# Kernel optimization log

Measured on AMD Instinct MI355X. Metric: run time of the kernel, lower is better.

## Reference

```python
import jax, jax.numpy as jnp
import numpy as np

B, N, D, H = 8, 4096, 256, 4
KP, KN = N // 16, N // 32
EPS = 1e-6

def _ln(x, g, b):
    m = jnp.mean(x, -1, keepdims=True)
    v = jnp.var(x, -1, keepdims=True)
    return (x - m) / jnp.sqrt(v + 1e-5) * g + b

def _cross_attn(q_in, kv_in, wq, wk, wv, wo, bo):
    # q_in [1,Nq,D], kv_in [1,Nk,D]
    Bq, Nq, Dm = q_in.shape
    Nk = kv_in.shape[1]
    dh = Dm // H
    q = (q_in @ wq).reshape(Bq, Nq, H, dh).transpose(0, 2, 1, 3)
    k = (kv_in @ wk).reshape(Bq, Nk, H, dh).transpose(0, 2, 1, 3)
    v = (kv_in @ wv).reshape(Bq, Nk, H, dh).transpose(0, 2, 1, 3)
    attn = jax.nn.softmax(jnp.einsum('bhqd,bhkd->bhqk', q, k) * (dh ** -0.5), axis=-1)
    out = jnp.einsum('bhqk,bhkd->bhqd', attn, v).transpose(0, 2, 1, 3).reshape(Bq, Nq, Dm)
    return out @ wo + bo

def setup_inputs():
    key = jax.random.key(0)
    ks = jax.random.split(key, 40)
    f32 = jnp.float32
    def w(i, shape, s):
        return s * jax.random.normal(ks[i], shape, f32)
    inp = {}
    inp['x'] = jax.random.normal(ks[0], (B, N, D), f32)
    inp['mask'] = (jax.random.randint(ks[1], (B, N), 0, 3) - 1).astype(jnp.int32)  # values in {-1,0,1}
    inp['pos_emb'] = 0.02 * jax.random.normal(ks[2], (1, N, D), f32)
    inp['sim_p_w'] = w(3, (D, D), 0.2); inp['sim_p_b'] = jnp.zeros((D,), f32)
    inp['sim_n_w'] = w(4, (D, D), 0.2); inp['sim_n_b'] = jnp.zeros((D,), f32)
    inp['adj_w'] = w(5, (D, D), 0.05)
    inp['gnn_p_w1'] = w(6, (D, D), 0.05); inp['gnn_p_w2'] = w(7, (D, D), 0.05)
    inp['gnn_n_w1'] = w(8, (D, D), 0.05); inp['gnn_n_w2'] = w(9, (D, D), 0.05)
    for i in range(1, 6):
        inp['ln%d_g' % i] = jnp.ones((D,), f32)
        inp['ln%d_b' % i] = jnp.zeros((D,), f32)
    names = ['i2q_wq', 'i2q_wk', 'i2q_wv', 'i2q_wo', 'q2i_wq', 'q2i_wk', 'q2i_wv', 'q2i_wo']
    for j, nme in enumerate(names):
        inp[nme] = w(10 + j, (D, D), 0.05)
    inp['i2q_bo'] = jnp.zeros((D,), f32)
    inp['q2i_bo'] = jnp.zeros((D,), f32)
    inp['mlp_w'] = w(20, (D, D), 0.05); inp['mlp_b'] = jnp.zeros((D,), f32)
    inp['g_i2t'] = 0.1 * jax.random.normal(ks[21], (1, 1, D), f32)
    inp['g_t2i'] = 0.1 * jax.random.normal(ks[22], (1, 1, D), f32)
    return inp

def reference(x, mask, pos_emb, sim_p_w, sim_p_b, sim_n_w, sim_n_b, adj_w,
              gnn_p_w1, gnn_p_w2, gnn_n_w1, gnn_n_w2,
              ln1_g, ln1_b, ln2_g, ln2_b, ln3_g, ln3_b, ln4_g, ln4_b, ln5_g, ln5_b,
              i2q_wq, i2q_wk, i2q_wv, i2q_wo, i2q_bo,
              q2i_wq, q2i_wk, q2i_wv, q2i_wo, q2i_bo,
              mlp_w, mlp_b, g_i2t, g_t2i):
    pos_mask = (mask == 1).astype(x.dtype)[..., None]    # [B,N,1]
    neg_mask = (mask == -1).astype(x.dtype)[..., None]
    pos_query = (x * pos_mask).sum(1, keepdims=True) / (pos_mask.sum(1, keepdims=True) + EPS)  # [B,1,D]
    neg_query = (x * neg_mask).sum(1, keepdims=True) / (neg_mask.sum(1, keepdims=True) + EPS)
    pos_sim = jax.nn.sigmoid(((x @ sim_p_w + sim_p_b) * pos_query).sum(-1))  # [B,N]
    neg_sim = jax.nn.sigmoid(((x @ sim_n_w + sim_n_b) * neg_query).sum(-1))
    weight_p, idx_p = jax.lax.top_k(pos_sim, KP)
    weight_n, idx_n = jax.lax.top_k(neg_sim, KN)
    scale = 1.0 / jnp.sqrt(jnp.asarray(D, x.dtype))

    def gcn(node, w1, w2):
        adj = jax.nn.softmax((node @ adj_w) @ node.T * scale, axis=-1)  # [K,K]
        h = jax.nn.relu(adj @ (node @ w1))
        return adj @ (h @ w2)

    def batch_forward(ip, wp, inn, wn, feat):
        node_p = feat[ip] * (wp > 0.6).astype(feat.dtype)[:, None]       # [KP,D]
        query_p = gcn(node_p, gnn_p_w1, gnn_p_w2) + pos_emb[0, ip]
        node_n = feat[inn] * (wn > 0.6).astype(feat.dtype)[:, None]      # [KN,D]
        query_n = gcn(node_n, gnn_n_w1, gnn_n_w2) + pos_emb[0, inn]
        query = jnp.concatenate([query_p, query_n], 0)[None]             # [1,KP+KN,D]
        featb = feat[None]                                               # [1,N,D]
        query = query + g_i2t * _cross_attn(_ln(query, ln1_g, ln1_b), _ln(featb, ln2_g, ln2_b),
                                            i2q_wq, i2q_wk, i2q_wv, i2q_wo, i2q_bo)
        featb = featb + g_t2i * _cross_attn(_ln(featb, ln3_g, ln3_b), _ln(query, ln4_g, ln4_b),
                                            q2i_wq, q2i_wk, q2i_wv, q2i_wo, q2i_bo)
        featb = featb + (_ln(featb, ln5_g, ln5_b) @ mlp_w + mlp_b)
        return featb

    out = jax.vmap(batch_forward)(idx_p, weight_p, idx_n, weight_n, x)   # [B,1,N,D]
    return out, pos_sim, neg_sim
```

## Files before the change

kernel.cpp:

```cpp
#include <hip/hip_runtime.h>

#define BB 8
#define NN 4096
#define DD 256
#define HH 4
#define DHH 64
#define KPP 256
#define KNN 128
#define SCH 64

typedef float f32x4 __attribute__((ext_vector_type(4)));
typedef short bf16x8 __attribute__((ext_vector_type(8)));
typedef short bf16x4 __attribute__((ext_vector_type(4)));

#define FLAG_TRANSB 1
#define FLAG_RELU   2

__device__ __forceinline__ float bf2f(unsigned short u){
  union { unsigned int i; float f; } v; v.i = ((unsigned int)u) << 16; return v.f;
}
__device__ __forceinline__ unsigned short f2bf(float f){
  union { float f; unsigned int i; } v; v.f = f;
  return (unsigned short)((v.i + 0x7FFFu + ((v.i >> 16) & 1u)) >> 16);
}
__device__ __forceinline__ void gload16(const void* g, void* l){
  __builtin_amdgcn_global_load_lds((const __attribute__((address_space(1))) void*)g,
                                   (__attribute__((address_space(3))) void*)l, 16, 0, 0);
}

__global__ __launch_bounds__(256) void stats_part(const float* __restrict__ x,
                                                  const int* __restrict__ mask,
                                                  float* __restrict__ part,
                                                  float* __restrict__ pcnt){
  int b = blockIdx.y, c = blockIdx.x, t = threadIdx.x;
  int w = t >> 6, lane = t & 63;
  const int R = NN / SCH;
  int n0 = c * R;
  const float* xb = x + ((long)b*NN + n0)*DD;
  const int* mb = mask + (long)b*NN + n0;
  float4 sp = {0.f,0.f,0.f,0.f}, sn = {0.f,0.f,0.f,0.f};
  int cp = 0, cn = 0;
  #pragma unroll 4
  for (int r = w; r < R; r += 4){
    int mv = mb[r];
    float4 v = ((const float4*)(xb + (long)r*DD))[lane];
    if (mv == 1){ sp.x += v.x; sp.y += v.y; sp.z += v.z; sp.w += v.w; cp++; }
    else if (mv == -1){ sn.x += v.x; sn.y += v.y; sn.z += v.z; sn.w += v.w; cn++; }
  }
  __shared__ float red[2][4][256];
  __shared__ int cnt[2][4];
  ((float4*)&red[0][w][0])[lane] = sp;
  ((float4*)&red[1][w][0])[lane] = sn;
  if (lane == 0){ cnt[0][w] = cp; cnt[1][w] = cn; }
  __syncthreads();
  float s0 = red[0][0][t]+red[0][1][t]+red[0][2][t]+red[0][3][t];
  float s1 = red[1][0][t]+red[1][1][t]+red[1][2][t]+red[1][3][t];
  part[(((long)(b*SCH+c)*2+0)*DD)+t] = s0;
  part[(((long)(b*SCH+c)*2+1)*DD)+t] = s1;
  if (t == 0){
    pcnt[(b*SCH+c)*2+0] = (float)(cnt[0][0]+cnt[0][1]+cnt[0][2]+cnt[0][3]);
    pcnt[(b*SCH+c)*2+1] = (float)(cnt[1][0]+cnt[1][1]+cnt[1][2]+cnt[1][3]);
  }
}

__global__ void stats_vec(const float* __restrict__ part, const float* __restrict__ pcnt,
                          const float* __restrict__ Wp, const float* __restrict__ bp,
                          const float* __restrict__ Wn, const float* __restrict__ bn,
                          float* __restrict__ vvec, float* __restrict__ cscal){
  int b = blockIdx.x, k = threadIdx.x;
  __shared__ float qp[256], qn[256], red[256];
  {
    float sp=0.f, sn=0.f, cp=0.f, cn=0.f;
    for (int c = 0; c < SCH; c++){
      sp += part[(((long)(b*SCH+c)*2+0)*DD)+k];
      sn += part[(((long)(b*SCH+c)*2+1)*DD)+k];
      cp += pcnt[(b*SCH+c)*2+0];
      cn += pcnt[(b*SCH+c)*2+1];
    }
    qp[k] = sp / (cp + 1e-6f);
    qn[k] = sn / (cn + 1e-6f);
  }
  __syncthreads();
  float vp = 0.f, vn = 0.f;
  for (int j = 0; j < DD; j++){ vp += Wp[(long)k*DD+j]*qp[j]; vn += Wn[(long)k*DD+j]*qn[j]; }
  vvec[(long)(b*2+0)*DD+k] = vp; vvec[(long)(b*2+1)*DD+k] = vn;
  red[k] = bp[k]*qp[k];
  __syncthreads();
  for (int s = 128; s > 0; s >>= 1){ if (k < s) red[k] += red[k+s]; __syncthreads(); }
  if (k == 0) cscal[b*2+0] = red[0];
  __syncthreads();
  red[k] = bn[k]*qn[k];
  __syncthreads();
  for (int s = 128; s > 0; s >>= 1){ if (k < s) red[k] += red[k+s]; __syncthreads(); }
  if (k == 0) cscal[b*2+1] = red[0];
}

__global__ void sim_norm_kernel(const float* __restrict__ x, const float* __restrict__ vvec,
                                const float* __restrict__ cscal,
                                float* __restrict__ simP, float* __restrict__ simN,
                                unsigned short* __restrict__ xhat){
  int b = blockIdx.y;
  int w = threadIdx.x >> 6, lane = threadIdx.x & 63;
  int n = blockIdx.x*4 + w;
  long row = (long)b*NN + n;
  const float4* xr = (const float4*)(x + row*DD);
  float4 xv = xr[lane];
  float4 a = ((const float4*)(vvec + (long)(b*2+0)*DD))[lane];
  float4 c = ((const float4*)(vvec + (long)(b*2+1)*DD))[lane];
  float sp = xv.x*a.x + xv.y*a.y + xv.z*a.z + xv.w*a.w;
  float sn = xv.x*c.x + xv.y*c.y + xv.z*c.z + xv.w*c.w;
  float s  = xv.x+xv.y+xv.z+xv.w;
  float q  = xv.x*xv.x+xv.y*xv.y+xv.z*xv.z+xv.w*xv.w;
  for (int off = 32; off; off >>= 1){
    sp += __shfl_xor(sp, off); sn += __shfl_xor(sn, off);
    s  += __shfl_xor(s, off);  q  += __shfl_xor(q, off);
  }
  float m = s*(1.f/256.f);
  float var = q*(1.f/256.f) - m*m;
  float rinv = rsqrtf(var + 1e-5f);
  ushort4 o;
  o.x = f2bf((xv.x-m)*rinv); o.y = f2bf((xv.y-m)*rinv);
  o.z = f2bf((xv.z-m)*rinv); o.w = f2bf((xv.w-m)*rinv);
  ((ushort4*)(xhat + row*DD))[lane] = o;
  if (lane == 0){
    float zp = sp + cscal[b*2+0], zn = sn + cscal[b*2+1];
    simP[row] = 1.f/(1.f+expf(-zp));
    simN[row] = 1.f/(1.f+expf(-zn));
  }
}

__global__ __launch_bounds__(256) void topk_radix(const float* __restrict__ simP,
                                                  const float* __restrict__ simN,
                                                  const float* __restrict__ x,
                                                  int* __restrict__ idxb, float* __restrict__ wb,
                                                  float* __restrict__ node){
  __shared__ unsigned int vals[4096];
  __shared__ unsigned int hist[4096];
  __shared__ unsigned short eql[4096];
  __shared__ unsigned int tsum[256];
  __shared__ unsigned int sB, sRem, sCG, sCnt, sEq;
  int id = blockIdx.x; int sgn = id & 1, b = id >> 1;
  int K = (sgn == 0) ? KPP : KNN;
  const float* s = (sgn == 0 ? simP : simN) + (long)b*NN;
  int t = threadIdx.x;
  if (t == 0){ sCG = 0; sCnt = 0; sEq = 0; }
  for (int i = t; i < 4096; i += 256){ vals[i] = __float_as_uint(s[i]); hist[i] = 0; }
  __syncthreads();

  auto find_thresh = [&](int NB, unsigned need){
    int per = NB >> 8;
    int base = t*per;
    unsigned local = 0;
    for (int j = 0; j < per; j++) local += hist[base+j];
    tsum[t] = local;
    __syncthreads();
    #pragma unroll
    for (int st = 1; st < 256; st <<= 1){
      unsigned v = (t + st < 256) ? tsum[t+st] : 0u;
      __syncthreads();
      tsum[t] += v;
      __syncthreads();
    }
    unsigned after = (t < 255) ? tsum[t+1] : 0u;
    if (after < need && after + local >= need){
      unsigned c = after;
      for (int j = per-1; j >= 0; j--){
        unsigned h = hist[base+j];
        c += h;
        if (c >= need){
          sB = (unsigned)(base+j);
          sRem = need - (c - h);
          atomicAdd(&sCG, c - h);
          break;
        }
      }
    }
    __syncthreads();
  };

  for (int i = t; i < 4096; i += 256) atomicAdd(&hist[vals[i] >> 20], 1u);
  __syncthreads();
  find_thresh(4096, (unsigned)K);
  unsigned B1 = sB, rem1 = sRem;
  __syncthreads();
  for (int i = t; i < 4096; i += 256) hist[i] = 0;
  __syncthreads();
  for (int i = t; i < 4096; i += 256){
    unsigned v = vals[i];
    if ((v >> 20) == B1) atomicAdd(&hist[(v >> 8) & 0xFFFu], 1u);
  }
  __syncthreads();
  find_thresh(4096, rem1);
  unsigned B2 = sB, rem2 = sRem;
  unsigned pre = (B1 << 12) | B2;
  __syncthreads();
  hist[t] = 0;
  __syncthreads();
  for (int i = t; i < 4096; i += 256){
    unsigned v = vals[i];
    if ((v >> 8) == pre) atomicAdd(&hist[v & 0xFFu], 1u);
  }
  __syncthreads();
  find_thresh(256, rem2);
  unsigned T = (pre << 8) | sB;
  unsigned cg = sCG;
  __syncthreads();
  hist[t] = 0;
  __syncthreads();

  int* oi = idxb + (long)id*256;
  float* ow = wb + (long)id*256;
  for (int i = t; i < 4096; i += 256){
    unsigned v = vals[i];
    if (v > T){
      unsigned p = atomicAdd(&sCnt, 1u);
      oi[p] = i; ow[p] = __uint_as_float(v);
      hist[p] = (unsigned)i; hist[256+p] = v;
    }
    else if (v == T){ unsigned e = atomicAdd(&sEq, 1u); eql[e] = (unsigned short)i; }
  }
  __syncthreads();
  int ne = K - (int)cg;
  int eqn = (int)sEq;
  for (int e = t; e < eqn; e += 256){
    int myi = eql[e]; int r = 0;
    for (int e2 = 0; e2 < eqn; e2++) r += (eql[e2] < myi);
    if (r < ne){
      oi[cg + r] = myi; ow[cg + r] = __uint_as_float(T);
      hist[cg + r] = (unsigned)myi; hist[256 + cg + r] = T;
    }
  }
  __syncthreads();
  int rbase = (sgn == 0) ? 0 : KPP;
  int lane = t & 63, rw = t >> 6;
  for (int i0 = 0; i0 < K; i0 += 4){
    int r = i0 + rw;
    int idx = (int)hist[r];
    float wv = __uint_as_float(hist[256 + r]);
    float4 vsel;
    if (wv > 0.6f) vsel = ((const float4*)(x + ((long)b*NN + idx)*DD))[lane];
    else vsel = (float4){0.f,0.f,0.f,0.f};
    ((float4*)(node + ((long)b*384 + rbase + r)*DD))[lane] = vsel;
  }
}

__global__ void softmax_dual(float* __restrict__ A0, int L0, int rpb0, long bs0, int rows0,
                             float* __restrict__ A1, int L1, int rpb1, long bs1, int rows1){
  int w = threadIdx.x >> 6, lane = threadIdx.x & 63;
  long row = (long)blockIdx.x*4 + w;
  float* A; int L, rpb; long bs;
  if (row < rows0){ A = A0; L = L0; rpb = rpb0; bs = bs0; }
  else { row -= rows0; if (row >= rows1) return; A = A1; L = L1; rpb = rpb1; bs = bs1; }
  int b = (int)(row / rpb), r = (int)(row % rpb);
  float* a = A + (long)b*bs + (long)r*L;
  int e = L >> 6;
  float vals[4]; float mx = -1e30f;
  for (int j = 0; j < e; j++){ vals[j] = a[lane*e+j]; mx = fmaxf(mx, vals[j]); }
  for (int off = 32; off; off >>= 1) mx = fmaxf(mx, __shfl_xor(mx, off));
  float sum = 0.f;
  for (int j = 0; j < e; j++){ vals[j] = expf(vals[j]-mx); sum += vals[j]; }
  for (int off = 32; off; off >>= 1) sum += __shfl_xor(sum, off);
  float rinv = 1.f/sum;
  for (int j = 0; j < e; j++) a[lane*e+j] = vals[j]*rinv;
}

__global__ void rownorm_kernel(const float* __restrict__ X, unsigned short* __restrict__ Y, int rows){
  int w = threadIdx.x >> 6, lane = threadIdx.x & 63;
  long row = (long)blockIdx.x*4 + w;
  if (row >= rows) return;
  const float4* xr = (const float4*)(X + row*DD);
  float4 xv = xr[lane];
  float s = xv.x+xv.y+xv.z+xv.w;
  float q = xv.x*xv.x+xv.y*xv.y+xv.z*xv.z+xv.w*xv.w;
  for (int off = 32; off; off >>= 1){ s += __shfl_xor(s, off); q += __shfl_xor(q, off); }
  float m = s*(1.f/256.f);
  float var = q*(1.f/256.f) - m*m;
  float rinv = rsqrtf(var + 1e-5f);
  ushort4 o;
  o.x = f2bf((xv.x-m)*rinv); o.y = f2bf((xv.y-m)*rinv);
  o.z = f2bf((xv.z-m)*rinv); o.w = f2bf((xv.w-m)*rinv);
  ((ushort4*)(Y + row*DD))[lane] = o;
}

struct FoldArgs { const float* W[9]; const float* g[9]; unsigned short* BT[9]; float sc[9]; };
struct BiasArgs { const float* W[7]; const float* b[7]; const float* addb[7]; float* out[7]; float sc[7]; };

__global__ void fold_w(FoldArgs fa){
  int m = blockIdx.y, tile = blockIdx.x, t = threadIdx.x;
  const float* W = fa.W[m]; const float* g = fa.g[m]; unsigned short* BT = fa.BT[m];
  float sc = fa.sc[m];
  __shared__ float T[64][65];
  int tn = (tile & 3)*64, tk = (tile >> 2)*64;
  #pragma unroll 4
  for (int p = 0; p < 16; p++){
    int kl = p*4 + (t >> 6), nl = t & 63;
    float v = W[(long)(tk+kl)*256 + tn + nl];
    if (g) v *= g[tk+kl];
    T[kl][nl] = v * sc;
  }
  __syncthreads();
  #pragma unroll 4
  for (int p = 0; p < 16; p++){
    int nl = p*4 + (t >> 6), kl = t & 63;
    BT[(long)(tn+nl)*256 + tk + kl] = f2bf(T[kl][nl]);
  }
}

__global__ void fold_b(BiasArgs ba){
  int m = blockIdx.x, n = threadIdx.x;
  const float* W = ba.W[m]; const float* b = ba.b[m];
  float s = (ba.addb[m] != nullptr) ? ba.addb[m][n] : 0.f;
  for (int k = 0; k < 256; k++) s += b[k]*W[(long)k*256+n];
  ba.out[m][n] = s * ba.sc[m];
}

struct GP {
  const float* A; long sAb; int lda;
  const float* B; long sBb; int ldb;
  float* C; long sCb; int ldc;
  const int* pidx; const float* pe;
  int M, N, K; float alpha; int flags;
};
struct GP4 { GP p[4]; };

__global__ __launch_bounds__(256) void gemm_multi(GP4 g4){
  GP p = g4.p[blockIdx.z >> 3];
  int b = blockIdx.z & 7;
  int m0 = blockIdx.y*64, n0 = blockIdx.x*64;
  if (m0 >= p.M || n0 >= p.N) return;
  __shared__ __align__(16) unsigned short As[64*40];
  __shared__ __align__(16) unsigned short Bs[64*40];
  const float* Ab = p.A + (long)b*p.sAb;
  const float* Bb = p.B + (long)b*p.sBb;
  int t = threadIdx.x;
  int w = t >> 6, lane = t & 63, lrowi = lane & 15, lquad = lane >> 4;
  int wm = w >> 1, wn = w & 1;
  f32x4 acc[2][2];
  #pragma unroll
  for (int i = 0; i < 2; i++)
    #pragma unroll
    for (int j = 0; j < 2; j++) acc[i][j] = (f32x4){0.f,0.f,0.f,0.f};
  int am = t >> 2, akq = t & 3;
  for (int k0 = 0; k0 < p.K; k0 += 32){
    {
      const float4* s4 = (const float4*)(Ab + (long)(m0+am)*p.lda + k0 + akq*8);
      float4 u = s4[0], vv = s4[1];
      unsigned short tmp[8];
      tmp[0]=f2bf(u.x); tmp[1]=f2bf(u.y); tmp[2]=f2bf(u.z); tmp[3]=f2bf(u.w);
      tmp[4]=f2bf(vv.x); tmp[5]=f2bf(vv.y); tmp[6]=f2bf(vv.z); tmp[7]=f2bf(vv.w);
      *(uint4*)(&As[am*40 + akq*8]) = *(uint4*)tmp;
    }
    if (p.flags & FLAG_TRANSB){
      const float4* s4 = (const float4*)(Bb + (long)(n0+am)*p.ldb + k0 + akq*8);
      float4 u = s4[0], vv = s4[1];
      unsigned short tmp[8];
      tmp[0]=f2bf(u.x); tmp[1]=f2bf(u.y); tmp[2]=f2bf(u.z); tmp[3]=f2bf(u.w);
      tmp[4]=f2bf(vv.x); tmp[5]=f2bf(vv.y); tmp[6]=f2bf(vv.z); tmp[7]=f2bf(vv.w);
      *(uint4*)(&Bs[am*40 + akq*8]) = *(uint4*)tmp;
    } else {
      int bn = t & 63, bkb = (t >> 6)*8;
      #pragma unroll
      for (int j = 0; j < 8; j++)
        Bs[bn*40 + bkb + j] = f2bf(Bb[(long)(k0+bkb+j)*p.ldb + n0 + bn]);
    }
    __syncthreads();
    bf16x8 af[2], bfr[2];
    #pragma unroll
    for (int i = 0; i < 2; i++)
      af[i] = *(const bf16x8*)(&As[(wm*32 + i*16 + lrowi)*40 + lquad*8]);
    #pragma unroll
    for (int j = 0; j < 2; j++)
      bfr[j] = *(const bf16x8*)(&Bs[(wn*32 + j*16 + lrowi)*40 + lquad*8]);
    #pragma unroll
    for (int i = 0; i < 2; i++)
      #pragma unroll
      for (int j = 0; j < 2; j++)
        acc[i][j] = __builtin_amdgcn_mfma_f32_16x16x32_bf16(af[i], bfr[j], acc[i][j], 0, 0, 0);
    __syncthreads();
  }
  float* Cb = p.C + (long)b*p.sCb;
  #pragma unroll
  for (int i = 0; i < 2; i++)
    #pragma unroll
    for (int j = 0; j < 2; j++){
      int col = n0 + wn*32 + j*16 + lrowi;
      #pragma unroll
      for (int r = 0; r < 4; r++){
        int row = m0 + wm*32 + i*16 + lquad*4 + r;
        float v = p.alpha*acc[i][j][r];
        if (p.flags & FLAG_RELU) v = fmaxf(v, 0.f);
        if (p.pidx != nullptr){
          int idx = p.pidx[b*512 + row];
          v += p.pe[(long)idx*256 + col];
        }
        Cb[(long)row*p.ldc + col] = v;
      }
    }
}

template<typename OT, bool RES, bool GATE>
__global__ __launch_bounds__(256) void gemm128(
    const unsigned short* __restrict__ A, long sAb,
    const unsigned short* __restrict__ BT,
    OT* __restrict__ C, long sCb, int ldc,
    const float* __restrict__ R, long sRb,
    const float* __restrict__ bias, const float* __restrict__ gate)
{
  __shared__ __align__(16) unsigned short As[4096];
  __shared__ __align__(16) unsigned short Bs[4096];
  int t = threadIdx.x;
  int w = t >> 6, lane = t & 63, lrowi = lane & 15, lquad = lane >> 4;
  int wm = w >> 1, wn = w & 1;
  int m0 = blockIdx.y*128, n0 = blockIdx.x*128;
  const unsigned short* Ab = A + (long)blockIdx.z*sAb + (long)m0*256;
  const unsigned short* Bb = BT + (long)n0*256;
  int g0 = t, g1 = 256 + t;
  int row0 = g0 >> 2, kq0 = g0 & 3;
  int row1 = g1 >> 2, kq1 = g1 & 3;
  f32x4 acc[4][4];
  #pragma unroll
  for (int i = 0; i < 4; i++)
    #pragma unroll
    for (int j = 0; j < 4; j++) acc[i][j] = (f32x4){0.f,0.f,0.f,0.f};

  for (int k0 = 0; k0 < 256; k0 += 32){
    gload16(Ab + (long)row0*256 + k0 + kq0*8, &As[g0*8]);
    gload16(Ab + (long)row1*256 + k0 + kq1*8, &As[g1*8]);
    gload16(Bb + (long)row0*256 + k0 + kq0*8, &Bs[g0*8]);
    gload16(Bb + (long)row1*256 + k0 + kq1*8, &Bs[g1*8]);
    __syncthreads();
    bf16x8 af[4], bfr[4];
    #pragma unroll
    for (int i = 0; i < 4; i++)
      af[i] = *(const bf16x8*)(&As[((wm*64 + i*16 + lrowi)*4 + lquad)*8]);
    #pragma unroll
    for (int j = 0; j < 4; j++)
      bfr[j] = *(const bf16x8*)(&Bs[((wn*64 + j*16 + lrowi)*4 + lquad)*8]);
    #pragma unroll
    for (int i = 0; i < 4; i++)
      #pragma unroll
      for (int j = 0; j < 4; j++)
        acc[i][j] = __builtin_amdgcn_mfma_f32_16x16x32_bf16(af[i], bfr[j], acc[i][j], 0, 0, 0);
    __syncthreads();
  }
  OT* Cb = C + (long)blockIdx.z*sCb;
  const float* Rb = RES ? (R + (long)blockIdx.z*sRb) : nullptr;
  #pragma unroll
  for (int j = 0; j < 4; j++){
    int col = n0 + wn*64 + j*16 + lrowi;
    float bv = bias[col];
    float gv = GATE ? gate[col] : 1.f;
    #pragma unroll
    for (int i = 0; i < 4; i++){
      #pragma unroll
      for (int r = 0; r < 4; r++){
        int row = m0 + wm*64 + i*16 + lquad*4 + r;
        float v = acc[i][j][r] + bv;
        if (GATE) v *= gv;
        if (RES) v += Rb[(long)row*256 + col];
        if constexpr (sizeof(OT) == 4) Cb[(long)row*ldc + col] = v;
        else                           Cb[(long)row*ldc + col] = f2bf(v);
      }
    }
  }
}

template<int NFRAG>
__global__ __launch_bounds__(256) void flash_kernel(
    const unsigned short* __restrict__ Q, long sQb, int ldq,
    const unsigned short* __restrict__ Kt, const unsigned short* __restrict__ Vt,
    long sKb, int ldkv,
    unsigned short* __restrict__ O, long sOb,
    float* __restrict__ Opart, float* __restrict__ Lpart,
    int Nq, int Nk, int nsplit)
{
  __shared__ __align__(16) unsigned short Kl[32*72];
  __shared__ __align__(16) unsigned short Vl[64*36];
  __shared__ __align__(16) unsigned short Pl[4*NFRAG*16*36];
  int b = blockIdx.z, h = blockIdx.y;
  int nqg = Nq / (64*NFRAG);
  int qg = blockIdx.x % nqg, split = blockIdx.x / nqg;
  int kchunk = Nk / nsplit;
  int kbeg = split*kchunk, kend = kbeg + kchunk;
  int t = threadIdx.x, w = t >> 6, lane = t & 63, lrowi = lane & 15, lquad = lane >> 4;
  int q0 = qg*(64*NFRAG) + w*(16*NFRAG);
  const unsigned short* Qb = Q + (long)b*sQb + h*DHH;
  const unsigned short* Kb = Kt + (long)b*sKb + h*DHH;
  const unsigned short* Vb = Vt + (long)b*sKb + h*DHH;
  bf16x8 qa[NFRAG][2];
  #pragma unroll
  for (int f = 0; f < NFRAG; f++)
    #pragma unroll
    for (int kt = 0; kt < 2; kt++)
      qa[f][kt] = *(const bf16x8*)(Qb + (long)(q0 + f*16 + lrowi)*ldq + kt*32 + lquad*8);

  f32x4 o[NFRAG][4];
  float psum[NFRAG][4];
  #pragma unroll
  for (int f = 0; f < NFRAG; f++)
    #pragma unroll
    for (int cj = 0; cj < 4; cj++){
      o[f][cj] = (f32x4){0.f,0.f,0.f,0.f};
      psum[f][cj] = 0.f;
    }
  int skq = t >> 3, sdq = (t & 7)*8;
  int skrow = ((skq & 1) << 4) | (skq >> 1);
  int vkq = t & 31, vdq = (t >> 5)*8;
  unsigned short* Pw = &Pl[w*(NFRAG*16*36)];

  for (int kt0 = kbeg; kt0 < kend; kt0 += 32){
    {
      uint4 kv = *(const uint4*)(Kb + (long)(kt0+skq)*ldkv + sdq);
      *(uint4*)(&Kl[skrow*72 + sdq]) = kv;
      uint4 vv = *(const uint4*)(Vb + (long)(kt0+vkq)*ldkv + vdq);
      const unsigned short* vp = (const unsigned short*)&vv;
      #pragma unroll
      for (int j = 0; j < 8; j++) Vl[(vdq+j)*36 + vkq] = vp[j];
    }
    __syncthreads();
    bf16x8 kb0 = *(const bf16x8*)(&Kl[(0*16+lrowi)*72 + lquad*8]);
    bf16x8 kb1 = *(const bf16x8*)(&Kl[(0*16+lrowi)*72 + 32 + lquad*8]);
    bf16x8 kb2 = *(const bf16x8*)(&Kl[(1*16+lrowi)*72 + lquad*8]);
    bf16x8 kb3 = *(const bf16x8*)(&Kl[(1*16+lrowi)*72 + 32 + lquad*8]);
    union { bf16x8 v8; bf16x4 v4[2]; } vbu[4];
    #pragma unroll
    for (int cj = 0; cj < 4; cj++){
      const unsigned short* vb = &Vl[(cj*16+lrowi)*36 + lquad*8];
      vbu[cj].v4[0] = *(const bf16x4*)vb;
      vbu[cj].v4[1] = *(const bf16x4*)(vb + 4);
    }
    #pragma unroll
    for (int f = 0; f < NFRAG; f++){
      f32x4 S0 = (f32x4){0.f,0.f,0.f,0.f}, S1 = (f32x4){0.f,0.f,0.f,0.f};
      S0 = __builtin_amdgcn_mfma_f32_16x16x32_bf16(qa[f][0], kb0, S0, 0, 0, 0);
      S0 = __builtin_amdgcn_mfma_f32_16x16x32_bf16(qa[f][1], kb1, S0, 0, 0, 0);
      S1 = __builtin_amdgcn_mfma_f32_16x16x32_bf16(qa[f][0], kb2, S1, 0, 0, 0);
      S1 = __builtin_amdgcn_mfma_f32_16x16x32_bf16(qa[f][1], kb3, S1, 0, 0, 0);
      unsigned short* Pf = Pw + f*(16*36);
      #pragma unroll
      for (int r = 0; r < 4; r++){
        float p0 = exp2f(S0[r]);
        float p1 = exp2f(S1[r]);
        psum[f][r] += p0 + p1;
        unsigned int pk;
        asm("v_cvt_pk_bf16_f32 %0, %1, %2" : "=v"(pk) : "v"(p0), "v"(p1));
        *(unsigned int*)(&Pf[(lquad*4+r)*36 + 2*lrowi]) = pk;
      }
    }
    __asm__ volatile("s_waitcnt lgkmcnt(0)" ::: "memory");
    #pragma unroll
    for (int f = 0; f < NFRAG; f++){
      const unsigned short* pp = &Pw[f*(16*36) + lrowi*36 + lquad*8];
      union { bf16x8 v8; bf16x4 v4[2]; } pa;
      pa.v4[0] = *(const bf16x4*)pp;
      pa.v4[1] = *(const bf16x4*)(pp + 4);
      #pragma unroll
      for (int cj = 0; cj < 4; cj++)
        o[f][cj] = __builtin_amdgcn_mfma_f32_16x16x32_bf16(pa.v8, vbu[cj].v8, o[f][cj], 0, 0, 0);
    }
    __syncthreads();
  }
  float lsum[NFRAG][4];
  #pragma unroll
  for (int f = 0; f < NFRAG; f++)
    #pragma unroll
    for (int r = 0; r < 4; r++){
      float s = psum[f][r];
      #pragma unroll
      for (int off = 1; off < 16; off <<= 1) s += __shfl_xor(s, off);
      lsum[f][r] = s;
    }
  if (nsplit > 1){
    int p = (b*HH + h)*nsplit + split;
    float* Op = Opart + (long)p*Nq*DHH;
    #pragma unroll
    for (int f = 0; f < NFRAG; f++)
      #pragma unroll
      for (int r = 0; r < 4; r++){
        int row = q0 + f*16 + lquad*4 + r;
        #pragma unroll
        for (int cj = 0; cj < 4; cj++)
          Op[(long)row*DHH + cj*16 + lrowi] = o[f][cj][r];
        if (lrowi == 0) Lpart[(long)p*Nq + row] = lsum[f][r];
      }
  } else {
    unsigned short* Ob = O + (long)b*sOb + h*DHH;
    #pragma unroll
    for (int f = 0; f < NFRAG; f++)
      #pragma unroll
      for (int r = 0; r < 4; r++){
        float rl = 1.f/lsum[f][r];
        int row = q0 + f*16 + lquad*4 + r;
        #pragma unroll
        for (int cj = 0; cj < 4; cj++)
          Ob[(long)row*DD + cj*16 + lrowi] = f2bf(o[f][cj][r]*rl);
      }
  }
}

__global__ void flash_combine(const float* __restrict__ Opart, const float* __restrict__ Lpart,
                              unsigned short* __restrict__ O, long sOb, int Nq, int nsplit){
  int gr = blockIdx.x*4 + (threadIdx.x >> 6);
  int d = threadIdx.x & 63;
  int bh = gr / Nq, row = gr % Nq;
  float accO = 0.f, accL = 0.f;
  for (int s = 0; s < nsplit; s++){
    long p = (long)bh*nsplit + s;
    accL += Lpart[p*Nq + row];
    accO += Opart[(p*Nq + row)*DHH + d];
  }
  int b = bh / HH, h = bh % HH;
  O[(long)b*sOb + (long)row*DD + h*DHH + d] = f2bf(accO/accL);
}

extern "C" void kernel_launch(void* const* d_in, const int* in_sizes, int n_in,
                              void* d_out, int out_size, void* d_ws, size_t ws_size,
                              hipStream_t stream) {
  (void)in_sizes; (void)n_in; (void)out_size; (void)ws_size;
  const float* x        = (const float*)d_in[0];
  const int*   mask     = (const int*)d_in[1];
  const float* pos_emb  = (const float*)d_in[2];
  const float* sim_p_w  = (const float*)d_in[3];
  const float* sim_p_b  = (const float*)d_in[4];
  const float* sim_n_w  = (const float*)d_in[5];
  const float* sim_n_b  = (const float*)d_in[6];
  const float* adj_w    = (const float*)d_in[7];
  const float* gnn_p_w1 = (const float*)d_in[8];
  const float* gnn_p_w2 = (const float*)d_in[9];
  const float* gnn_n_w1 = (const float*)d_in[10];
  const float* gnn_n_w2 = (const float*)d_in[11];
  const float* ln1_g = (const float*)d_in[12]; const float* ln1_b = (const float*)d_in[13];
  const float* ln2_g = (const float*)d_in[14]; const float* ln2_b = (const float*)d_in[15];
  const float* ln3_g = (const float*)d_in[16]; const float* ln3_b = (const float*)d_in[17];
  const float* ln4_g = (const float*)d_in[18]; const float* ln4_b = (const float*)d_in[19];
  const float* ln5_g = (const float*)d_in[20]; const float* ln5_b = (const float*)d_in[21];
  const float* i2q_wq = (const float*)d_in[22];
  const float* i2q_wk = (const float*)d_in[23];
  const float* i2q_wv = (const float*)d_in[24];
  const float* i2q_wo = (const float*)d_in[25];
  const float* q2i_wq = (const float*)d_in[26];
  const float* q2i_wk = (const float*)d_in[27];
  const float* q2i_wv = (const float*)d_in[28];
  const float* q2i_wo = (const float*)d_in[29];
  const float* i2q_bo = (const float*)d_in[30];
  const float* q2i_bo = (const float*)d_in[31];
  const float* mlp_w  = (const float*)d_in[32];
  const float* mlp_b  = (const float*)d_in[33];
  const float* g_i2t  = (const float*)d_in[34];
  const float* g_t2i  = (const float*)d_in[35];

  float* out  = (float*)d_out;
  float* simP = out + (size_t)BB*NN*DD;
  float* simN = simP + (size_t)BB*NN;

  char* w8 = (char*)d_ws;
  size_t off = 0;
  auto take = [&](size_t bytes)->void*{
    void* p = (void*)(w8 + off);
    off += (bytes + 255) & ~(size_t)255;
    return p;
  };
  float* part   = (float*)take((size_t)BB*SCH*2*DD*4);
  float* pcnt   = (float*)take((size_t)BB*SCH*2*4);
  float* vvec   = (float*)take((size_t)BB*2*DD*4);
  float* cscal  = (float*)take((size_t)BB*2*4);
  int*   idxb   = (int*)take((size_t)BB*2*256*4);
  float* wb     = (float*)take((size_t)BB*2*256*4);
  float* node   = (float*)take((size_t)BB*384*DD*4);
  float* gA     = (float*)take((size_t)BB*384*DD*4);
  float* gadjP  = (float*)take((size_t)BB*256*256*4);
  float* gadjN  = (float*)take((size_t)BB*128*128*4);
  float* query  = (float*)take((size_t)BB*384*DD*4);
  float* query2 = (float*)take((size_t)BB*384*DD*4);
  unsigned short* xhatq  = (unsigned short*)take((size_t)BB*384*DD*2);
  unsigned short* qh     = (unsigned short*)take((size_t)BB*384*DD*2);
  unsigned short* attnZ  = (unsigned short*)take((size_t)BB*384*DD*2);
  unsigned short* xhatq2 = (unsigned short*)take((size_t)BB*384*DD*2);
  unsigned short* kv2    = (unsigned short*)take((size_t)BB*384*512*2);
  unsigned short* xhat   = (unsigned short*)take((size_t)BB*NN*DD*2);
  unsigned short* kvq    = (unsigned short*)take((size_t)BB*NN*768*2);
  float* featb2 = (float*)take((size_t)BB*NN*DD*4);
  float* Lpart  = (float*)take((size_t)BB*HH*8*384*4);
  unsigned short* wTq1  = (unsigned short*)take((size_t)65536*2);
  unsigned short* wTbig = (unsigned short*)take((size_t)3*65536*2);
  unsigned short* wTkv2 = (unsigned short*)take((size_t)2*65536*2);
  unsigned short* wTmlp = (unsigned short*)take((size_t)65536*2);
  unsigned short* wTo1  = (unsigned short*)take((size_t)65536*2);
  unsigned short* wTo2  = (unsigned short*)take((size_t)65536*2);
  float* biasQ1  = (float*)take(256*4);
  float* biasBig = (float*)take(768*4);
  float* biasKV2 = (float*)take(512*4);
  float* biasMlp = (float*)take(256*4);
  float* t1 = query;
  float* t2 = query2;
  float* t3 = gA;
  unsigned short* attn2 = xhat;
  unsigned short* xhat5 = kvq;
  float* Opart = featb2;

  const long sQ  = 384L*DD;
  const long sX  = (long)NN*DD;
  const float* NF = nullptr;

  const float QS = 0.125f * 1.44269504088896f;

  FoldArgs fa;
  fa.W[0]=i2q_wq; fa.g[0]=ln1_g; fa.BT[0]=wTq1;            fa.sc[0]=QS;
  fa.W[1]=i2q_wk; fa.g[1]=ln2_g; fa.BT[1]=wTbig;           fa.sc[1]=1.f;
  fa.W[2]=i2q_wv; fa.g[2]=ln2_g; fa.BT[2]=wTbig + 256*256; fa.sc[2]=1.f;
  fa.W[3]=q2i_wq; fa.g[3]=ln3_g; fa.BT[3]=wTbig + 512*256; fa.sc[3]=QS;
  fa.W[4]=q2i_wk; fa.g[4]=ln4_g; fa.BT[4]=wTkv2;           fa.sc[4]=1.f;
  fa.W[5]=q2i_wv; fa.g[5]=ln4_g; fa.BT[5]=wTkv2 + 256*256; fa.sc[5]=1.f;
  fa.W[6]=mlp_w;  fa.g[6]=ln5_g; fa.BT[6]=wTmlp;           fa.sc[6]=1.f;
  fa.W[7]=i2q_wo; fa.g[7]=nullptr; fa.BT[7]=wTo1;          fa.sc[7]=1.f;
  fa.W[8]=q2i_wo; fa.g[8]=nullptr; fa.BT[8]=wTo2;          fa.sc[8]=1.f;
  fold_w<<<dim3(16,9), 256, 0, stream>>>(fa);
  BiasArgs ba;
  ba.W[0]=i2q_wq; ba.b[0]=ln1_b; ba.addb[0]=nullptr; ba.out[0]=biasQ1;     ba.sc[0]=QS;
  ba.W[1]=i2q_wk; ba.b[1]=ln2_b; ba.addb[1]=nullptr; ba.out[1]=biasBig;    ba.sc[1]=1.f;
  ba.W[2]=i2q_wv; ba.b[2]=ln2_b; ba.addb[2]=nullptr; ba.out[2]=biasBig+256; ba.sc[2]=1.f;
  ba.W[3]=q2i_wq; ba.b[3]=ln3_b; ba.addb[3]=nullptr; ba.out[3]=biasBig+512; ba.sc[3]=QS;
  ba.W[4]=q2i_wk; ba.b[4]=ln4_b; ba.addb[4]=nullptr; ba.out[4]=biasKV2;    ba.sc[4]=1.f;
  ba.W[5]=q2i_wv; ba.b[5]=ln4_b; ba.addb[5]=nullptr; ba.out[5]=biasKV2+256; ba.sc[5]=1.f;
  ba.W[6]=mlp_w;  ba.b[6]=ln5_b; ba.addb[6]=mlp_b;   ba.out[6]=biasMlp;    ba.sc[6]=1.f;
  fold_b<<<7, 256, 0, stream>>>(ba);

  stats_part<<<dim3(SCH, BB), 256, 0, stream>>>(x, mask, part, pcnt);
  stats_vec<<<BB, 256, 0, stream>>>(part, pcnt, sim_p_w, sim_p_b, sim_n_w, sim_n_b, vvec, cscal);
  sim_norm_kernel<<<dim3(NN/4, BB), 256, 0, stream>>>(x, vvec, cscal, simP, simN, xhat);
  topk_radix<<<2*BB, 256, 0, stream>>>(simP, simN, x, idxb, wb, node);

  GP z = {};
  {
    GP4 g;
    g.p[0] = { node, 384L*DD, 256, adj_w, 0, 256, gA, 384L*DD, 256, nullptr, nullptr, 384, 256, 256, 1.f, 0 };
    g.p[1] = { node, 384L*DD, 256, gnn_p_w1, 0, 256, t1, 384L*DD, 256, nullptr, nullptr, 256, 256, 256, 1.f, 0 };
    g.p[2] = { node + 256L*DD, 384L*DD, 256, gnn_n_w1, 0, 256, t1 + 256L*DD, 384L*DD, 256, nullptr, nullptr, 128, 256, 256, 1.f, 0 };
    g.p[3] = z;
    gemm_multi<<<dim3(4,6,3*BB), 256, 0, stream>>>(g);
  }
  {
    GP4 g;
    g.p[0] = { gA, 384L*DD, 256, node, 384L*DD, 256, gadjP, 65536L, 256, nullptr, nullptr, 256, 256, 256, 0.0625f, FLAG_TRANSB };
    g.p[1] = { gA + 256L*DD, 384L*DD, 256, node + 256L*DD, 384L*DD, 256, gadjN, 16384L, 128, nullptr, nullptr, 128, 128, 256, 0.0625f, FLAG_TRANSB };
    g.p[2] = z; g.p[3] = z;
    gemm_multi<<<dim3(4,4,2*BB), 256, 0, stream>>>(g);
  }
  softmax_dual<<<768, 256, 0, stream>>>(gadjP, 256, 256, 65536L, BB*256,
                                        gadjN, 128, 128, 16384L, BB*128);
  {
    GP4 g;
    g.p[0] = { gadjP, 65536L, 256, t1, 384L*DD, 256, t2, 384L*DD, 256, nullptr, nullptr, 256, 256, 256, 1.f, FLAG_RELU };
    g.p[1] = { gadjN, 16384L, 128, t1 + 256L*DD, 384L*DD, 256, t2 + 256L*DD, 384L*DD, 256, nullptr, nullptr, 128, 256, 128, 1.f, FLAG_RELU };
    g.p[2] = z; g.p[3] = z;
    gemm_multi<<<dim3(4,4,2*BB), 256, 0, stream>>>(g);
  }
  {
    GP4 g;
    g.p[0] = { t2, 384L*DD, 256, gnn_p_w2, 0, 256, t3, 384L*DD, 256, nullptr, nullptr, 256, 256, 256, 1.f, 0 };
    g.p[1] = { t2 + 256L*DD, 384L*DD, 256, gnn_n_w2, 0, 256, t3 + 256L*DD, 384L*DD, 256, nullptr, nullptr, 128, 256, 256, 1.f, 0 };
    g.p[2] = z; g.p[3] = z;
    gemm_multi<<<dim3(4,4,2*BB), 256, 0, stream>>>(g);
  }
  {
    GP4 g;
    g.p[0] = { gadjP, 65536L, 256, t3, 384L*DD, 256, query, 384L*DD, 256, idxb, pos_emb, 256, 256, 256, 1.f, 0 };
    g.p[1] = { gadjN, 16384L, 128, t3 + 256L*DD, 384L*DD, 256, query + 256L*DD, 384L*DD, 256, idxb + 256, pos_emb, 128, 256, 128, 1.f, 0 };
    g.p[2] = z; g.p[3] = z;
    gemm_multi<<<dim3(4,4,2*BB), 256, 0, stream>>>(g);
  }

  rownorm_kernel<<<BB*384/4, 256, 0, stream>>>(query, xhatq, BB*384);

  gemm128<unsigned short,false,false><<<dim3(2,3,BB),256,0,stream>>>(
      xhatq, sQ, wTq1, qh, sQ, 256, NF, 0, biasQ1, NF);
  gemm128<unsigned short,false,false><<<dim3(6,32,BB),256,0,stream>>>(
      xhat, sX, wTbig, kvq, (long)NN*768, 768, NF, 0, biasBig, NF);
  flash_kernel<3><<<dim3(2*8, HH, BB), 256, 0, stream>>>(
      qh, sQ, 256, kvq, kvq + 256, (long)NN*768, 768,
      attnZ, sQ, Opart, Lpart, 384, NN, 8);
  flash_combine<<<BB*HH*384/4, 256, 0, stream>>>(Opart, Lpart, attnZ, sQ, 384, 8);
  gemm128<float,true,true><<<dim3(2,3,BB),256,0,stream>>>(
      attnZ, sQ, wTo1, query2, sQ, 256, query, sQ, i2q_bo, g_i2t);

  rownorm_kernel<<<BB*384/4, 256, 0, stream>>>(query2, xhatq2, BB*384);
  gemm128<unsigned short,false,false><<<dim3(4,3,BB),256,0,stream>>>(
      xhatq2, sQ, wTkv2, kv2, 384L*512, 512, NF, 0, biasKV2, NF);
  flash_kernel<2><<<dim3(32, HH, BB), 256, 0, stream>>>(
      kvq + 512, (long)NN*768, 768, kv2, kv2 + 256, 384L*512, 512,
      attn2, sX, nullptr, nullptr, NN, 384, 1);
  gemm128<float,true,true><<<dim3(2,32,BB),256,0,stream>>>(
      attn2, sX, wTo2, featb2, sX, 256, x, sX, q2i_bo, g_t2i);

  rownorm_kernel<<<BB*NN/4, 256, 0, stream>>>(featb2, xhat5, BB*NN);
  gemm128<float,true,false><<<dim3(2,32,BB),256,0,stream>>>(
      xhat5, sX, wTmlp, out, sX, 256, featb2, sX, biasMlp, NF);
}
```

Baseline: 485.7 us.

## Double-buffer LDS tiles in GEMM and flash-attention kernels to overlap loads

Both the 128x128 GEMM and the flash-attention kernel now use two LDS buffers per tile. The next K-slice is issued (gload16 direct-to-LDS in the GEMM, register prefetch in flash) before computing on the current one. This is meant to hide global-memory latency behind the MFMA work. Explicit waitcnt plus raw s_barrier replace __syncthreads, and the doubled LDS footprint may reduce occupancy.

```diff
diff --git a/kernel.cpp b/kernel.cpp
--- a/kernel.cpp
+++ b/kernel.cpp
@@ -406,8 +406,8 @@
     const float* __restrict__ R, long sRb,
     const float* __restrict__ bias, const float* __restrict__ gate)
 {
-  __shared__ __align__(16) unsigned short As[4096];
-  __shared__ __align__(16) unsigned short Bs[4096];
+  __shared__ __align__(16) unsigned short As[2][4096];
+  __shared__ __align__(16) unsigned short Bs[2][4096];
   int t = threadIdx.x;
   int w = t >> 6, lane = t & 63, lrowi = lane & 15, lquad = lane >> 4;
   int wm = w >> 1, wn = w & 1;
@@ -423,25 +423,37 @@
     #pragma unroll
     for (int j = 0; j < 4; j++) acc[i][j] = (f32x4){0.f,0.f,0.f,0.f};
 
-  for (int k0 = 0; k0 < 256; k0 += 32){
-    gload16(Ab + (long)row0*256 + k0 + kq0*8, &As[g0*8]);
-    gload16(Ab + (long)row1*256 + k0 + kq1*8, &As[g1*8]);
-    gload16(Bb + (long)row0*256 + k0 + kq0*8, &Bs[g0*8]);
-    gload16(Bb + (long)row1*256 + k0 + kq1*8, &Bs[g1*8]);
-    __syncthreads();
+  auto stage = [&](int buf, int k0){
+    gload16(Ab + (long)row0*256 + k0 + kq0*8, &As[buf][g0*8]);
+    gload16(Ab + (long)row1*256 + k0 + kq1*8, &As[buf][g1*8]);
+    gload16(Bb + (long)row0*256 + k0 + kq0*8, &Bs[buf][g0*8]);
+    gload16(Bb + (long)row1*256 + k0 + kq1*8, &Bs[buf][g1*8]);
+  };
+
+  stage(0, 0);
+  for (int it = 0; it < 8; it++){
+    int cur = it & 1;
+    if (it < 7){
+      stage(cur ^ 1, (it+1)*32);
+      __asm__ volatile("s_waitcnt vmcnt(4)" ::: "memory");
+    } else {
+      __asm__ volatile("s_waitcnt vmcnt(0)" ::: "memory");
+    }
+    __builtin_amdgcn_s_barrier();
     bf16x8 af[4], bfr[4];
     #pragma unroll
     for (int i = 0; i < 4; i++)
-      af[i] = *(const bf16x8*)(&As[((wm*64 + i*16 + lrowi)*4 + lquad)*8]);
+      af[i] = *(const bf16x8*)(&As[cur][((wm*64 + i*16 + lrowi)*4 + lquad)*8]);
     #pragma unroll
     for (int j = 0; j < 4; j++)
-      bfr[j] = *(const bf16x8*)(&Bs[((wn*64 + j*16 + lrowi)*4 + lquad)*8]);
+      bfr[j] = *(const bf16x8*)(&Bs[cur][((wn*64 + j*16 + lrowi)*4 + lquad)*8]);
     #pragma unroll
     for (int i = 0; i < 4; i++)
       #pragma unroll
       for (int j = 0; j < 4; j++)
         acc[i][j] = __builtin_amdgcn_mfma_f32_16x16x32_bf16(af[i], bfr[j], acc[i][j], 0, 0, 0);
-    __syncthreads();
+    __asm__ volatile("s_waitcnt lgkmcnt(0)" ::: "memory");
+    __builtin_amdgcn_s_barrier();
   }
   OT* Cb = C + (long)blockIdx.z*sCb;
   const float* Rb = RES ? (R + (long)blockIdx.z*sRb) : nullptr;
@@ -474,14 +486,15 @@
     float* __restrict__ Opart, float* __restrict__ Lpart,
     int Nq, int Nk, int nsplit)
 {
-  __shared__ __align__(16) unsigned short Kl[32*72];
-  __shared__ __align__(16) unsigned short Vl[64*36];
+  __shared__ __align__(16) unsigned short Kl[2][32*72];
+  __shared__ __align__(16) unsigned short Vl[2][64*36];
   __shared__ __align__(16) unsigned short Pl[4*NFRAG*16*36];
   int b = blockIdx.z, h = blockIdx.y;
   int nqg = Nq / (64*NFRAG);
   int qg = blockIdx.x % nqg, split = blockIdx.x / nqg;
   int kchunk = Nk / nsplit;
-  int kbeg = split*kchunk, kend = kbeg + kchunk;
+  int kbeg = split*kchunk;
+  int nt = kchunk >> 5;
   int t = threadIdx.x, w = t >> 6, lane = t & 63, lrowi = lane & 15, lquad = lane >> 4;
   int q0 = qg*(64*NFRAG) + w*(16*NFRAG);
   const unsigned short* Qb = Q + (long)b*sQb + h*DHH;
@@ -508,24 +521,32 @@
   int vkq = t & 31, vdq = (t >> 5)*8;
   unsigned short* Pw = &Pl[w*(NFRAG*16*36)];
 
-  for (int kt0 = kbeg; kt0 < kend; kt0 += 32){
-    {
-      uint4 kv = *(const uint4*)(Kb + (long)(kt0+skq)*ldkv + sdq);
-      *(uint4*)(&Kl[skrow*72 + sdq]) = kv;
-      uint4 vv = *(const uint4*)(Vb + (long)(kt0+vkq)*ldkv + vdq);
-      const unsigned short* vp = (const unsigned short*)&vv;
-      #pragma unroll
-      for (int j = 0; j < 8; j++) Vl[(vdq+j)*36 + vkq] = vp[j];
-    }
-    __syncthreads();
-    bf16x8 kb0 = *(const bf16x8*)(&Kl[(0*16+lrowi)*72 + lquad*8]);
-    bf16x8 kb1 = *(const bf16x8*)(&Kl[(0*16+lrowi)*72 + 32 + lquad*8]);
-    bf16x8 kb2 = *(const bf16x8*)(&Kl[(1*16+lrowi)*72 + lquad*8]);
-    bf16x8 kb3 = *(const bf16x8*)(&Kl[(1*16+lrowi)*72 + 32 + lquad*8]);
+  uint4 kreg = *(const uint4*)(Kb + (long)(kbeg+skq)*ldkv + sdq);
+  uint4 vreg = *(const uint4*)(Vb + (long)(kbeg+vkq)*ldkv + vdq);
+  {
+    *(uint4*)(&Kl[0][skrow*72 + sdq]) = kreg;
+    const unsigned short* vp = (const unsigned short*)&vreg;
+    #pragma unroll
+    for (int j = 0; j < 8; j++) Vl[0][(vdq+j)*36 + vkq] = vp[j];
+  }
+
+  for (int it = 0; it < nt; it++){
+    int cur = it & 1;
+    if (it + 1 < nt){
+      int kt0 = kbeg + (it+1)*32;
+      kreg = *(const uint4*)(Kb + (long)(kt0+skq)*ldkv + sdq);
+      vreg = *(const uint4*)(Vb + (long)(kt0+vkq)*ldkv + vdq);
+    }
+    __asm__ volatile("s_waitcnt lgkmcnt(0)" ::: "memory");
+    __builtin_amdgcn_s_barrier();
+    bf16x8 kb0 = *(const bf16x8*)(&Kl[cur][(0*16+lrowi)*72 + lquad*8]);
+    bf16x8 kb1 = *(const bf16x8*)(&Kl[cur][(0*16+lrowi)*72 + 32 + lquad*8]);
+    bf16x8 kb2 = *(const bf16x8*)(&Kl[cur][(1*16+lrowi)*72 + lquad*8]);
+    bf16x8 kb3 = *(const bf16x8*)(&Kl[cur][(1*16+lrowi)*72 + 32 + lquad*8]);
     union { bf16x8 v8; bf16x4 v4[2]; } vbu[4];
     #pragma unroll
     for (int cj = 0; cj < 4; cj++){
-      const unsigned short* vb = &Vl[(cj*16+lrowi)*36 + lquad*8];
+      const unsigned short* vb = &Vl[cur][(cj*16+lrowi)*36 + lquad*8];
       vbu[cj].v4[0] = *(const bf16x4*)vb;
       vbu[cj].v4[1] = *(const bf16x4*)(vb + 4);
     }
@@ -558,7 +579,14 @@
       for (int cj = 0; cj < 4; cj++)
         o[f][cj] = __builtin_amdgcn_mfma_f32_16x16x32_bf16(pa.v8, vbu[cj].v8, o[f][cj], 0, 0, 0);
     }
-    __syncthreads();
+    __asm__ volatile("s_waitcnt lgkmcnt(0)" ::: "memory");
+    __builtin_amdgcn_s_barrier();
+    if (it + 1 < nt){
+      *(uint4*)(&Kl[cur^1][skrow*72 + sdq]) = kreg;
+      const unsigned short* vp = (const unsigned short*)&vreg;
+      #pragma unroll
+      for (int j = 0; j < 8; j++) Vl[cur^1][(vdq+j)*36 + vkq] = vp[j];
+    }
   }
   float lsum[NFRAG][4];
   #pragma unroll
```

Result: no change. 483.2 us (-0.5%).

## Double-buffer LDS tiles in gemm128 and raise wave priority around attention MFMAs

Applied to the files above, without the earlier changes.

The 128x128 GEMM kernel now keeps two LDS buffers and issues the global loads for the next K-slice before computing the current one. It uses explicit vmcnt/lgkmcnt waits and raw barriers in place of two __syncthreads per iteration, so load latency can overlap with MFMA work. In the attention kernel, s_setprio is raised around the MFMA blocks to favour waves issuing matrix work. The cost is twice the LDS use in the GEMM, which may reduce occupancy, and correctness now relies on the hand-placed waitcnt counts matching the async gload16 behaviour.

```diff
diff --git a/kernel.cpp b/kernel.cpp
--- a/kernel.cpp
+++ b/kernel.cpp
@@ -406,8 +406,8 @@
     const float* __restrict__ R, long sRb,
     const float* __restrict__ bias, const float* __restrict__ gate)
 {
-  __shared__ __align__(16) unsigned short As[4096];
-  __shared__ __align__(16) unsigned short Bs[4096];
+  __shared__ __align__(16) unsigned short As[2][4096];
+  __shared__ __align__(16) unsigned short Bs[2][4096];
   int t = threadIdx.x;
   int w = t >> 6, lane = t & 63, lrowi = lane & 15, lquad = lane >> 4;
   int wm = w >> 1, wn = w & 1;
@@ -423,25 +423,37 @@
     #pragma unroll
     for (int j = 0; j < 4; j++) acc[i][j] = (f32x4){0.f,0.f,0.f,0.f};
 
-  for (int k0 = 0; k0 < 256; k0 += 32){
-    gload16(Ab + (long)row0*256 + k0 + kq0*8, &As[g0*8]);
-    gload16(Ab + (long)row1*256 + k0 + kq1*8, &As[g1*8]);
-    gload16(Bb + (long)row0*256 + k0 + kq0*8, &Bs[g0*8]);
-    gload16(Bb + (long)row1*256 + k0 + kq1*8, &Bs[g1*8]);
-    __syncthreads();
+  auto stage = [&](int buf, int k0){
+    gload16(Ab + (long)row0*256 + k0 + kq0*8, &As[buf][g0*8]);
+    gload16(Ab + (long)row1*256 + k0 + kq1*8, &As[buf][g1*8]);
+    gload16(Bb + (long)row0*256 + k0 + kq0*8, &Bs[buf][g0*8]);
+    gload16(Bb + (long)row1*256 + k0 + kq1*8, &Bs[buf][g1*8]);
+  };
+
+  stage(0, 0);
+  for (int it = 0; it < 8; it++){
+    int cur = it & 1;
+    if (it < 7){
+      stage(cur ^ 1, (it+1)*32);
+      __asm__ volatile("s_waitcnt vmcnt(4)" ::: "memory");
+    } else {
+      __asm__ volatile("s_waitcnt vmcnt(0)" ::: "memory");
+    }
+    __builtin_amdgcn_s_barrier();
     bf16x8 af[4], bfr[4];
     #pragma unroll
     for (int i = 0; i < 4; i++)
-      af[i] = *(const bf16x8*)(&As[((wm*64 + i*16 + lrowi)*4 + lquad)*8]);
+      af[i] = *(const bf16x8*)(&As[cur][((wm*64 + i*16 + lrowi)*4 + lquad)*8]);
     #pragma unroll
     for (int j = 0; j < 4; j++)
-      bfr[j] = *(const bf16x8*)(&Bs[((wn*64 + j*16 + lrowi)*4 + lquad)*8]);
+      bfr[j] = *(const bf16x8*)(&Bs[cur][((wn*64 + j*16 + lrowi)*4 + lquad)*8]);
     #pragma unroll
     for (int i = 0; i < 4; i++)
       #pragma unroll
       for (int j = 0; j < 4; j++)
         acc[i][j] = __builtin_amdgcn_mfma_f32_16x16x32_bf16(af[i], bfr[j], acc[i][j], 0, 0, 0);
-    __syncthreads();
+    __asm__ volatile("s_waitcnt lgkmcnt(0)" ::: "memory");
+    __builtin_amdgcn_s_barrier();
   }
   OT* Cb = C + (long)blockIdx.z*sCb;
   const float* Rb = RES ? (R + (long)blockIdx.z*sRb) : nullptr;
@@ -532,10 +544,12 @@
     #pragma unroll
     for (int f = 0; f < NFRAG; f++){
       f32x4 S0 = (f32x4){0.f,0.f,0.f,0.f}, S1 = (f32x4){0.f,0.f,0.f,0.f};
+      __builtin_amdgcn_s_setprio(1);
       S0 = __builtin_amdgcn_mfma_f32_16x16x32_bf16(qa[f][0], kb0, S0, 0, 0, 0);
       S0 = __builtin_amdgcn_mfma_f32_16x16x32_bf16(qa[f][1], kb1, S0, 0, 0, 0);
       S1 = __builtin_amdgcn_mfma_f32_16x16x32_bf16(qa[f][0], kb2, S1, 0, 0, 0);
       S1 = __builtin_amdgcn_mfma_f32_16x16x32_bf16(qa[f][1], kb3, S1, 0, 0, 0);
+      __builtin_amdgcn_s_setprio(0);
       unsigned short* Pf = Pw + f*(16*36);
       #pragma unroll
       for (int r = 0; r < 4; r++){
@@ -554,9 +568,11 @@
       union { bf16x8 v8; bf16x4 v4[2]; } pa;
       pa.v4[0] = *(const bf16x4*)pp;
       pa.v4[1] = *(const bf16x4*)(pp + 4);
+      __builtin_amdgcn_s_setprio(1);
       #pragma unroll
       for (int cj = 0; cj < 4; cj++)
         o[f][cj] = __builtin_amdgcn_mfma_f32_16x16x32_bf16(pa.v8, vbu[cj].v8, o[f][cj], 0, 0, 0);
+      __builtin_amdgcn_s_setprio(0);
     }
     __syncthreads();
   }
```

After: 477.0 us. Within noise of the previous version (-1.8%).
